# Kernel tuning notes

Measured on AMD Instinct MI355X. Metric: run time of the kernel, lower is better.

## Reference

```python
import jax, jax.numpy as jnp
import numpy as np

B, H, L, D, LBL = 512, 64, 528, 32, 10
NI = 64          # number of interval breakpoints
W = 128          # vf MLP width
N_STEPS = 256    # fixed Tsit5 steps over [t0, t1]

# Tsit5 Butcher tableau
C2, C3, C4, C5, C6 = 0.161, 0.327, 0.9, 0.9800255409045097, 1.0
A21 = 0.161
A31, A32 = -0.008480655492356989, 0.335480655492357
A41, A42, A43 = 2.8971530571054935, -6.359448489975075, 4.3622954328695815
A51, A52, A53, A54 = 5.325864828439257, -11.748883564062828, 7.4955393428898365, -0.09249506636175525
A61, A62, A63, A64, A65 = 5.86145544294642, -12.92096931784711, 8.159367898576159, -0.071584973281401, -0.028269050394068383
B1, B2, B3, B4, B5, B6 = 0.09646076681806523, 0.01, 0.4798896504144996, 1.379008574103742, -3.290069515436081, 2.324710524099774


def _linear_init(k, out_dim, in_dim):
    lim = 1.0 / np.sqrt(in_dim)
    kw, kb = jax.random.split(k)
    w = jax.random.uniform(kw, (out_dim, in_dim), jnp.float32, -lim, lim)
    b = jax.random.uniform(kb, (out_dim,), jnp.float32, -lim, lim)
    return w, b


def setup_inputs() -> dict:
    key = jax.random.key(0)
    ks = jax.random.split(key, 8)
    ts = jnp.linspace(0.0, 1.0, 129, dtype=jnp.float32)
    logsig = 0.1 * jax.random.normal(ks[0], (B, NI + 1, L + 1), jnp.float32)
    x0 = jax.random.normal(ks[1], (B, D), jnp.float32)
    intervals = jnp.linspace(0.0, 1.0, NI, dtype=jnp.float32)
    vf_w0, vf_b0 = _linear_init(ks[2], W, H)
    vf_w1, vf_b1 = _linear_init(ks[3], W, W)
    vf_w2, vf_b2 = _linear_init(ks[4], W, W)
    vf_w3, vf_b3 = _linear_init(ks[5], H * L, W)
    l1_w, l1_b = _linear_init(ks[6], H, D)
    l2_w, l2_b = _linear_init(ks[7], LBL, H)
    return dict(ts=ts, logsig=logsig, x0=x0, intervals=intervals,
                vf_w0=vf_w0, vf_b0=vf_b0, vf_w1=vf_w1, vf_b1=vf_b1,
                vf_w2=vf_w2, vf_b2=vf_b2, vf_w3=vf_w3, vf_b3=vf_b3,
                l1_w=l1_w, l1_b=l1_b, l2_w=l2_w, l2_b=l2_b)


def reference(ts, logsig, x0, intervals,
              vf_w0, vf_b0, vf_w1, vf_b1, vf_w2, vf_b2, vf_w3, vf_b3,
              l1_w, l1_b, l2_w, l2_b):
    Bn = x0.shape[0]
    Hn = l1_w.shape[0]
    Ln = vf_b3.shape[0] // Hn

    def vf(y):  # y: (B, H) -> (B, H, L)
        h = jax.nn.silu(y @ vf_w0.T + vf_b0)
        h = jax.nn.silu(h @ vf_w1.T + vf_b1)
        h = jax.nn.silu(h @ vf_w2.T + vf_b2)
        out = jnp.tanh(h @ vf_w3.T + vf_b3)
        return out.reshape(Bn, Hn, Ln)

    def func(t, y):
        idx = jnp.searchsorted(intervals, t)
        sig = logsig[:, idx, 1:]          # (B, L)
        return jnp.einsum('bhl,bl->bh', vf(y), sig)

    t0, t1 = ts[0], ts[-1]
    dt = (t1 - t0) / N_STEPS

    def step(y, i):
        t = t0 + i * dt
        k1 = func(t, y)
        k2 = func(t + C2 * dt, y + dt * (A21 * k1))
        k3 = func(t + C3 * dt, y + dt * (A31 * k1 + A32 * k2))
        k4 = func(t + C4 * dt, y + dt * (A41 * k1 + A42 * k2 + A43 * k3))
        k5 = func(t + C5 * dt, y + dt * (A51 * k1 + A52 * k2 + A53 * k3 + A54 * k4))
        k6 = func(t + C6 * dt, y + dt * (A61 * k1 + A62 * k2 + A63 * k3 + A64 * k4 + A65 * k5))
        y_new = y + dt * (B1 * k1 + B2 * k2 + B3 * k3 + B4 * k4 + B5 * k5 + B6 * k6)
        return y_new, None

    y0 = x0 @ l1_w.T + l1_b
    yT, _ = jax.lax.scan(step, y0, jnp.arange(N_STEPS, dtype=jnp.float32))
    return jax.nn.softmax(yT @ l2_w.T + l2_b, axis=-1)
```

## Files before the change

kernel.cpp:

```cpp
#include <hip/hip_runtime.h>
#include <stdint.h>

#define NBLK 256
#define NTHR 512

typedef __attribute__((ext_vector_type(8))) short short8;
typedef __attribute__((ext_vector_type(4))) float float4_;

#define WS_BAR  0
#define WS_HDNF 16384
#define WS_KF   (16384 + 131072)

#define LOADC(p)    __hip_atomic_load((p),  __ATOMIC_RELAXED, __HIP_MEMORY_SCOPE_SYSTEM)
#define STOREC(p,v) __hip_atomic_store((p), (v), __ATOMIC_RELAXED, __HIP_MEMORY_SCOPE_SYSTEM)

__device__ __forceinline__ unsigned short f2bf(float x) {
  union { float f; unsigned u; } v; v.f = x;
  return (unsigned short)((v.u + 0x7fffu + ((v.u >> 16) & 1u)) >> 16);
}
__device__ __forceinline__ float fast_exp(float x) {
  return __builtin_amdgcn_exp2f(x * 1.4426950408889634f);
}
__device__ __forceinline__ float fast_tanh(float x) {
  float e = __builtin_amdgcn_exp2f(x * 2.8853900817779268f);
  return fmaf(-2.0f, __builtin_amdgcn_rcpf(e + 1.0f), 1.0f);
}
__device__ __forceinline__ float fast_silu(float x) {
  float e = fast_exp(-x);
  return x * __builtin_amdgcn_rcpf(1.0f + e);
}

__device__ __forceinline__ void rgbar(unsigned* bar, int h, int Rg, unsigned bn) {
  __syncthreads();
  if (threadIdx.x == 0) {
    unsigned* base = bar + 32 * (32 + Rg * 16);
    unsigned* leaf = base + 32 * (h & 7);
    unsigned* root = base + 32 * 8;
    unsigned* gen  = base + 32 * 9;
    unsigned a = __hip_atomic_fetch_add(leaf, 1u, __ATOMIC_RELAXED, __HIP_MEMORY_SCOPE_SYSTEM);
    if (a == 8u * bn - 1u) {
      unsigned r = __hip_atomic_fetch_add(root, 1u, __ATOMIC_RELAXED, __HIP_MEMORY_SCOPE_SYSTEM);
      if (r == 8u * bn - 1u) STOREC(gen, bn);
    }
    while (LOADC(gen) < bn) __builtin_amdgcn_s_sleep(1);
  }
  __syncthreads();
}

template<int SIN>
__device__ __forceinline__ void rk_stage(
    int stepi, int sg, int g, int h, int Rg, int R,
    float (&kh)[6], float& y, float t0v, float dtv,
    unsigned char* ws, unsigned* BAR, unsigned& rseq,
    const float* logsig, const float* w0, const float* b0,
    const float* w1, const float* b1, const float* w2, const float* b2,
    unsigned short* w3lds, float* b3lds, float* intv,
    float (*yst)[64], float (*hb1)[128], float (*hb2)[128],
    unsigned short (*hdnS)[128], int* sidxp) {
  const int tid = threadIdx.x;
  const int lane = tid & 63, wv = tid >> 6;
  const int col = lane & 15, qd = lane >> 4;
  unsigned* HDNF = (unsigned*)(ws + WS_HDNF);
  float* KF  = (float*)(ws + WS_KF);

  if (sg > 0 && tid < 128) {
    const float* KFr = KF + ((sg & 1) ^ 1) * 32768;
    constexpr int pi = (SIN == 0) ? 5 : SIN - 1;
    kh[pi] = LOADC(&KFr[(size_t)(2 * g + (tid >> 6)) * 64 + (tid & 63)]);
  }
  if (tid < 128) {
    float ystv;
    if constexpr (SIN == 0) {
      if (sg > 0) {
        y += dtv * (0.09646076681806523f * kh[0] + 0.01f * kh[1]
                  + 0.4798896504144996f * kh[2] + 1.379008574103742f * kh[3]
                  - 3.290069515436081f * kh[4] + 2.324710524099774f * kh[5]);
      }
      ystv = y;
    } else if constexpr (SIN == 1) {
      ystv = y + dtv * (0.161f * kh[0]);
    } else if constexpr (SIN == 2) {
      ystv = y + dtv * (-0.008480655492356989f * kh[0] + 0.335480655492357f * kh[1]);
    } else if constexpr (SIN == 3) {
      ystv = y + dtv * (2.8971530571054935f * kh[0] - 6.359448489975075f * kh[1]
                      + 4.3622954328695815f * kh[2]);
    } else if constexpr (SIN == 4) {
      ystv = y + dtv * (5.325864828439257f * kh[0] - 11.748883564062828f * kh[1]
                      + 7.4955393428898365f * kh[2] - 0.09249506636175525f * kh[3]);
    } else {
      ystv = y + dtv * (5.86145544294642f * kh[0] - 12.92096931784711f * kh[1]
                      + 8.159367898576159f * kh[2] - 0.071584973281401f * kh[3]
                      - 0.028269050394068383f * kh[4]);
    }
    yst[tid >> 6][tid & 63] = ystv;
  }
  {
    float tb = __fadd_rn(t0v, __fmul_rn((float)stepi, dtv));
    float t_cur;
    if constexpr (SIN == 0) t_cur = tb;
    else {
      constexpr float cS = (SIN == 1) ? 0.161f : (SIN == 2) ? 0.327f : (SIN == 3) ? 0.9f
                         : (SIN == 4) ? 0.9800255409045097f : 1.0f;
      t_cur = __fadd_rn(tb, __fmul_rn(cS, dtv));
    }
    if (tid < 64) {
      unsigned long long m1 = __ballot(intv[tid] < t_cur);
      if (tid == 0) *sidxp = (int)__popcll(m1);
    }
  }
  __syncthreads();
  const int idx = *sidxp;

  if (tid < 256) {
    const int row = tid >> 7, j = tid & 127;
    const float4_* wr = (const float4_*)(w0 + (size_t)j * 64);
    float ac[4] = {b0[j], 0.0f, 0.0f, 0.0f};
    #pragma unroll
    for (int i4 = 0; i4 < 16; ++i4) {
      float4_ wvv = wr[i4];
      float s = fmaf(yst[row][4*i4+0], wvv[0], yst[row][4*i4+1] * wvv[1]);
      s = fmaf(yst[row][4*i4+2], wvv[2], s);
      s = fmaf(yst[row][4*i4+3], wvv[3], s);
      ac[i4 & 3] += s;
    }
    hb1[row][j] = fast_silu((ac[0] + ac[1]) + (ac[2] + ac[3]));
  }
  __syncthreads();
  if (tid < 256) {
    const int row = tid >> 7, j = tid & 127;
    const float4_* wr = (const float4_*)(w1 + (size_t)j * 128);
    float ac[4] = {b1[j], 0.0f, 0.0f, 0.0f};
    #pragma unroll
    for (int i4 = 0; i4 < 32; ++i4) {
      float4_ wvv = wr[i4];
      float s = fmaf(hb1[row][4*i4+0], wvv[0], hb1[row][4*i4+1] * wvv[1]);
      s = fmaf(hb1[row][4*i4+2], wvv[2], s);
      s = fmaf(hb1[row][4*i4+3], wvv[3], s);
      ac[i4 & 3] += s;
    }
    hb2[row][j] = fast_silu((ac[0] + ac[1]) + (ac[2] + ac[3]));
  }
  __syncthreads();
  if (tid < 256) {
    const int row = tid >> 7, j = tid & 127;
    const float4_* wr = (const float4_*)(w2 + (size_t)j * 128);
    float ac[4] = {b2[j], 0.0f, 0.0f, 0.0f};
    #pragma unroll
    for (int i4 = 0; i4 < 32; ++i4) {
      float4_ wvv = wr[i4];
      float s = fmaf(hb2[row][4*i4+0], wvv[0], hb2[row][4*i4+1] * wvv[1]);
      s = fmaf(hb2[row][4*i4+2], wvv[2], s);
      s = fmaf(hb2[row][4*i4+3], wvv[3], s);
      ac[i4 & 3] += s;
    }
    hdnS[row][j] = f2bf(fast_silu((ac[0] + ac[1]) + (ac[2] + ac[3])));
  }
  __syncthreads();
  if (tid < 128) {
    const int row = tid >> 6, u = tid & 63;
    const int lb = 2 * h + row;
    const int tile = lb >> 4, colp = lb & 15;
    const int j0 = 2 * u;
    const int kb = j0 >> 5, qdp = (j0 >> 3) & 3, jj = j0 & 7;
    unsigned v = (unsigned)hdnS[row][j0] | ((unsigned)hdnS[row][j0 + 1] << 16);
    unsigned i16 = (unsigned)((Rg * 32 + tile * 4 + kb) * 512 + qdp * 128 + colp * 8 + jj);
    STOREC(&HDNF[i16 >> 1], v);
  }
  ++rseq; rgbar(BAR, h, Rg, rseq);

  {
    const unsigned long long* H64 = (const unsigned long long*)HDNF;
    union { unsigned long long u[2]; short8 s; } af[4];
    #pragma unroll
    for (int kb = 0; kb < 4; ++kb) {
      const unsigned i16 = (unsigned)((Rg * 32 + wv * 4 + kb) * 512 + lane * 8);
      af[kb].u[0] = LOADC(&H64[i16 >> 2]);
      af[kb].u[1] = LOADC(&H64[(i16 >> 2) + 1]);
    }
    const float* sp0 = logsig + (size_t)(R + wv * 16 + qd * 4) * 34385 + (size_t)idx * 529 + 1;
    const float* sp1 = sp0 + 34385;
    const float* sp2 = sp0 + 2 * 34385;
    const float* sp3 = sp0 + 3 * 34385;
    float kp[4] = {0.0f, 0.0f, 0.0f, 0.0f};
    #pragma unroll 2
    for (int nt = 0; nt < 33; ++nt) {
      const int l = nt * 16 + col;
      const float bv = b3lds[l];
      float4_ acc; acc[0] = bv; acc[1] = bv; acc[2] = bv; acc[3] = bv;
      #pragma unroll
      for (int kb = 0; kb < 4; ++kb) {
        const short8 bf = *(const short8*)(w3lds + ((nt * 4 + kb) * 64 + lane) * 8);
        acc = __builtin_amdgcn_mfma_f32_16x16x32_bf16(af[kb].s, bf, acc, 0, 0, 0);
      }
      kp[0] = fmaf(fast_tanh(acc[0]), sp0[l], kp[0]);
      kp[1] = fmaf(fast_tanh(acc[1]), sp1[l], kp[1]);
      kp[2] = fmaf(fast_tanh(acc[2]), sp2[l], kp[2]);
      kp[3] = fmaf(fast_tanh(acc[3]), sp3[l], kp[3]);
    }
    #pragma unroll
    for (int r = 0; r < 4; ++r) {
      float v = kp[r];
      v += __shfl_xor(v, 1); v += __shfl_xor(v, 2);
      v += __shfl_xor(v, 4); v += __shfl_xor(v, 8);
      kp[r] = v;
    }
    if (col == 0) {
      float* KFw = KF + (sg & 1) * 32768;
      #pragma unroll
      for (int r = 0; r < 4; ++r)
        STOREC(&KFw[(size_t)(R + wv * 16 + qd * 4 + r) * 64 + h], kp[r]);
    }
  }
  ++rseq; rgbar(BAR, h, Rg, rseq);
}

__global__ void __launch_bounds__(NTHR, 2)
rde_kernel(const float* __restrict__ ts, const float* __restrict__ logsig,
           const float* __restrict__ x0, const float* __restrict__ intervals,
           const float* __restrict__ w0, const float* __restrict__ b0,
           const float* __restrict__ w1, const float* __restrict__ b1,
           const float* __restrict__ w2, const float* __restrict__ b2,
           const float* __restrict__ w3, const float* __restrict__ b3,
           const float* __restrict__ l1w, const float* __restrict__ l1b,
           const float* __restrict__ l2w, const float* __restrict__ l2b,
           float* out, unsigned char* ws) {
  const int tid = threadIdx.x;
  const int g = blockIdx.x;
  const int h = g & 63;
  const int Rg = g >> 6;
  const int R = Rg * 128;
  unsigned* BAR = (unsigned*)(ws + WS_BAR);
  unsigned rseq = 0;

  __shared__ __attribute__((aligned(16))) unsigned short w3lds[67584];
  __shared__ float b3lds[528];
  __shared__ float intv[64];
  __shared__ float yst[2][64];
  __shared__ float hb1[2][128];
  __shared__ float hb2[2][128];
  __shared__ __attribute__((aligned(8))) unsigned short hdnS[2][128];
  __shared__ int sidx;

  if (tid < 64) intv[tid] = intervals[tid];
  for (int e = tid; e < 528; e += NTHR) b3lds[e] = b3[(size_t)h * 528 + e];

  for (int e = tid; e < 8448; e += NTHR) {
    const int ln = e & 63, kb = (e >> 6) & 3, nt = e >> 8;
    const float* src = w3 + ((size_t)(h * 528 + nt * 16 + (ln & 15))) * 128 + kb * 32 + (ln >> 4) * 8;
    union { unsigned short s[8]; short8 v; } p;
    #pragma unroll
    for (int j = 0; j < 8; ++j) p.s[j] = f2bf(src[j]);
    *(short8*)(w3lds + e * 8) = p.v;
  }

  float y = 0.0f, kh[6];
  #pragma unroll
  for (int i = 0; i < 6; ++i) kh[i] = 0.0f;
  if (tid < 128) {
    const int row = tid >> 6, hh = tid & 63;
    float acc = l1b[hh];
    const float4_* xr = (const float4_*)(x0 + (size_t)(2 * g + row) * 32);
    const float4_* wr = (const float4_*)(l1w + (size_t)hh * 32);
    #pragma unroll
    for (int d = 0; d < 8; ++d) {
      float4_ xv = xr[d], wvv = wr[d];
      acc = fmaf(xv[0], wvv[0], acc); acc = fmaf(xv[1], wvv[1], acc);
      acc = fmaf(xv[2], wvv[2], acc); acc = fmaf(xv[3], wvv[3], acc);
    }
    y = acc;
  }
  const float t0v = ts[0];
  const float dtv = (ts[128] - t0v) * (1.0f / 256.0f);
  __syncthreads();

  for (int stepi = 0; stepi < 256; ++stepi) {
    const int sg = stepi * 6;
    rk_stage<0>(stepi, sg + 0, g, h, Rg, R, kh, y, t0v, dtv, ws, BAR, rseq,
                logsig, w0, b0, w1, b1, w2, b2, w3lds, b3lds, intv, yst, hb1, hb2, hdnS, &sidx);
    rk_stage<1>(stepi, sg + 1, g, h, Rg, R, kh, y, t0v, dtv, ws, BAR, rseq,
                logsig, w0, b0, w1, b1, w2, b2, w3lds, b3lds, intv, yst, hb1, hb2, hdnS, &sidx);
    rk_stage<2>(stepi, sg + 2, g, h, Rg, R, kh, y, t0v, dtv, ws, BAR, rseq,
                logsig, w0, b0, w1, b1, w2, b2, w3lds, b3lds, intv, yst, hb1, hb2, hdnS, &sidx);
    rk_stage<3>(stepi, sg + 3, g, h, Rg, R, kh, y, t0v, dtv, ws, BAR, rseq,
                logsig, w0, b0, w1, b1, w2, b2, w3lds, b3lds, intv, yst, hb1, hb2, hdnS, &sidx);
    rk_stage<4>(stepi, sg + 4, g, h, Rg, R, kh, y, t0v, dtv, ws, BAR, rseq,
                logsig, w0, b0, w1, b1, w2, b2, w3lds, b3lds, intv, yst, hb1, hb2, hdnS, &sidx);
    rk_stage<5>(stepi, sg + 5, g, h, Rg, R, kh, y, t0v, dtv, ws, BAR, rseq,
                logsig, w0, b0, w1, b1, w2, b2, w3lds, b3lds, intv, yst, hb1, hb2, hdnS, &sidx);
  }

  {
    float* KF = (float*)(ws + WS_KF);
    if (tid < 128) {
      const int row = tid >> 6, hh = tid & 63;
      kh[5] = LOADC(&KF[(size_t)32768 + (size_t)(2 * g + row) * 64 + hh]);
      y += dtv * (0.09646076681806523f * kh[0] + 0.01f * kh[1]
                + 0.4798896504144996f * kh[2] + 1.379008574103742f * kh[3]
                - 3.290069515436081f * kh[4] + 2.324710524099774f * kh[5]);
      yst[row][hh] = y;
    }
    __syncthreads();
    if (tid < 20) {
      const int row = tid / 10, c = tid % 10;
      float acc = l2b[c];
      const float* wr = l2w + c * 64;
      #pragma unroll
      for (int i2 = 0; i2 < 64; ++i2) acc = fmaf(yst[row][i2], wr[i2], acc);
      hb1[row][c] = acc;
    }
    __syncthreads();
    if (tid < 2) {
      const int row = tid;
      float mx = -1e30f;
      for (int c = 0; c < 10; ++c) mx = fmaxf(mx, hb1[row][c]);
      float ev[10], den = 0.0f;
      for (int c = 0; c < 10; ++c) { ev[c] = expf(hb1[row][c] - mx); den += ev[c]; }
      const float rd = 1.0f / den;
      for (int c = 0; c < 10; ++c) out[(size_t)(2 * g + row) * 10 + c] = ev[c] * rd;
    }
  }
}

extern "C" void kernel_launch(void* const* d_in, const int* in_sizes, int n_in,
                              void* d_out, int out_size, void* d_ws, size_t ws_size,
                              hipStream_t stream) {
  (void)in_sizes; (void)n_in; (void)out_size; (void)ws_size;
  const float* ts        = (const float*)d_in[0];
  const float* logsig    = (const float*)d_in[1];
  const float* x0        = (const float*)d_in[2];
  const float* intervals = (const float*)d_in[3];
  const float* w0        = (const float*)d_in[4];
  const float* b0        = (const float*)d_in[5];
  const float* w1        = (const float*)d_in[6];
  const float* b1        = (const float*)d_in[7];
  const float* w2        = (const float*)d_in[8];
  const float* b2        = (const float*)d_in[9];
  const float* w3        = (const float*)d_in[10];
  const float* b3        = (const float*)d_in[11];
  const float* l1w       = (const float*)d_in[12];
  const float* l1b       = (const float*)d_in[13];
  const float* l2w       = (const float*)d_in[14];
  const float* l2b       = (const float*)d_in[15];
  float* out = (float*)d_out;
  unsigned char* ws = (unsigned char*)d_ws;

  hipMemsetAsync(d_ws, 0, 12288, stream);

  void* args[] = { &ts, &logsig, &x0, &intervals, &w0, &b0, &w1, &b1,
                   &w2, &b2, &w3, &b3, &l1w, &l1b, &l2w, &l2b, &out, &ws };
  hipLaunchCooperativeKernel((void*)rde_kernel, dim3(NBLK), dim3(NTHR), args, 0, stream);
}
```

Baseline: 36.38 ms.

## Keep MLP hidden-layer weights in registers and split dot products across all threads

The w1 and w2 rows each thread needs are loaded once into registers before the time loop, so the global/L2 weight reads inside every RK stage go away. The first three MLP layers now use all 512 threads, with each output split into two half-dot-products joined by a cross-lane shuffle. Block-to-(row group, head) mapping is also permuted, likely to place blocks sharing a barrier group together. The trade-off is higher register pressure, which could cause spills under the 2-blocks-per-CU launch bound, plus a shuffle per layer.

```diff
diff --git a/kernel.cpp b/kernel.cpp
--- a/kernel.cpp
+++ b/kernel.cpp
@@ -49,24 +49,26 @@
 
 template<int SIN>
 __device__ __forceinline__ void rk_stage(
-    int stepi, int sg, int g, int h, int Rg, int R,
+    int stepi, int sg, int h, int Rg, int R, int r0,
     float (&kh)[6], float& y, float t0v, float dtv,
+    const float4_ (&wr1)[16], const float4_ (&wr2)[16],
+    float b0r, float b1r, float b2r,
     unsigned char* ws, unsigned* BAR, unsigned& rseq,
-    const float* logsig, const float* w0, const float* b0,
-    const float* w1, const float* b1, const float* w2, const float* b2,
+    const float* logsig, const float* w0,
     unsigned short* w3lds, float* b3lds, float* intv,
     float (*yst)[64], float (*hb1)[128], float (*hb2)[128],
     unsigned short (*hdnS)[128], int* sidxp) {
   const int tid = threadIdx.x;
   const int lane = tid & 63, wv = tid >> 6;
   const int col = lane & 15, qd = lane >> 4;
+  const int mrow = tid >> 8, mj = ((tid >> 6) & 3) * 32 + (tid & 31), mhalf = (tid >> 5) & 1;
   unsigned* HDNF = (unsigned*)(ws + WS_HDNF);
   float* KF  = (float*)(ws + WS_KF);
 
   if (sg > 0 && tid < 128) {
     const float* KFr = KF + ((sg & 1) ^ 1) * 32768;
     constexpr int pi = (SIN == 0) ? 5 : SIN - 1;
-    kh[pi] = LOADC(&KFr[(size_t)(2 * g + (tid >> 6)) * 64 + (tid & 63)]);
+    kh[pi] = LOADC(&KFr[(size_t)(r0 + (tid >> 6)) * 64 + (tid & 63)]);
   }
   if (tid < 128) {
     float ystv;
@@ -111,49 +113,53 @@
   __syncthreads();
   const int idx = *sidxp;
 
-  if (tid < 256) {
-    const int row = tid >> 7, j = tid & 127;
-    const float4_* wr = (const float4_*)(w0 + (size_t)j * 64);
-    float ac[4] = {b0[j], 0.0f, 0.0f, 0.0f};
+  {
+    const float4_* wrp = (const float4_*)(w0 + (size_t)mj * 64 + mhalf * 32);
+    const float* yp = &yst[mrow][mhalf * 32];
+    float ac0 = 0.0f, ac1 = 0.0f;
+    #pragma unroll
+    for (int i4 = 0; i4 < 8; ++i4) {
+      float4_ wvv = wrp[i4];
+      float s = fmaf(yp[4*i4+0], wvv[0], yp[4*i4+1] * wvv[1]);
+      s = fmaf(yp[4*i4+2], wvv[2], s);
+      s = fmaf(yp[4*i4+3], wvv[3], s);
+      if (i4 & 1) ac1 += s; else ac0 += s;
+    }
+    float v = ac0 + ac1;
+    v += __shfl_xor(v, 32);
+    if (mhalf == 0) hb1[mrow][mj] = fast_silu(v + b0r);
+  }
+  __syncthreads();
+  {
+    const float* hp = &hb1[mrow][mhalf * 64];
+    float ac0 = 0.0f, ac1 = 0.0f;
     #pragma unroll
     for (int i4 = 0; i4 < 16; ++i4) {
-      float4_ wvv = wr[i4];
-      float s = fmaf(yst[row][4*i4+0], wvv[0], yst[row][4*i4+1] * wvv[1]);
-      s = fmaf(yst[row][4*i4+2], wvv[2], s);
-      s = fmaf(yst[row][4*i4+3], wvv[3], s);
-      ac[i4 & 3] += s;
-    }
-    hb1[row][j] = fast_silu((ac[0] + ac[1]) + (ac[2] + ac[3]));
-  }
-  __syncthreads();
-  if (tid < 256) {
-    const int row = tid >> 7, j = tid & 127;
-    const float4_* wr = (const float4_*)(w1 + (size_t)j * 128);
-    float ac[4] = {b1[j], 0.0f, 0.0f, 0.0f};
-    #pragma unroll
-    for (int i4 = 0; i4 < 32; ++i4) {
-      float4_ wvv = wr[i4];
-      float s = fmaf(hb1[row][4*i4+0], wvv[0], hb1[row][4*i4+1] * wvv[1]);
-      s = fmaf(hb1[row][4*i4+2], wvv[2], s);
-      s = fmaf(hb1[row][4*i4+3], wvv[3], s);
-      ac[i4 & 3] += s;
-    }
-    hb2[row][j] = fast_silu((ac[0] + ac[1]) + (ac[2] + ac[3]));
-  }
-  __syncthreads();
-  if (tid < 256) {
-    const int row = tid >> 7, j = tid & 127;
-    const float4_* wr = (const float4_*)(w2 + (size_t)j * 128);
-    float ac[4] = {b2[j], 0.0f, 0.0f, 0.0f};
-    #pragma unroll
-    for (int i4 = 0; i4 < 32; ++i4) {
-      float4_ wvv = wr[i4];
-      float s = fmaf(hb2[row][4*i4+0], wvv[0], hb2[row][4*i4+1] * wvv[1]);
-      s = fmaf(hb2[row][4*i4+2], wvv[2], s);
-      s = fmaf(hb2[row][4*i4+3], wvv[3], s);
-      ac[i4 & 3] += s;
-    }
-    hdnS[row][j] = f2bf(fast_silu((ac[0] + ac[1]) + (ac[2] + ac[3])));
+      float4_ wvv = wr1[i4];
+      float s = fmaf(hp[4*i4+0], wvv[0], hp[4*i4+1] * wvv[1]);
+      s = fmaf(hp[4*i4+2], wvv[2], s);
+      s = fmaf(hp[4*i4+3], wvv[3], s);
+      if (i4 & 1) ac1 += s; else ac0 += s;
+    }
+    float v = ac0 + ac1;
+    v += __shfl_xor(v, 32);
+    if (mhalf == 0) hb2[mrow][mj] = fast_silu(v + b1r);
+  }
+  __syncthreads();
+  {
+    const float* hp = &hb2[mrow][mhalf * 64];
+    float ac0 = 0.0f, ac1 = 0.0f;
+    #pragma unroll
+    for (int i4 = 0; i4 < 16; ++i4) {
+      float4_ wvv = wr2[i4];
+      float s = fmaf(hp[4*i4+0], wvv[0], hp[4*i4+1] * wvv[1]);
+      s = fmaf(hp[4*i4+2], wvv[2], s);
+      s = fmaf(hp[4*i4+3], wvv[3], s);
+      if (i4 & 1) ac1 += s; else ac0 += s;
+    }
+    float v = ac0 + ac1;
+    v += __shfl_xor(v, 32);
+    if (mhalf == 0) hdnS[mrow][mj] = f2bf(fast_silu(v + b2r));
   }
   __syncthreads();
   if (tid < 128) {
@@ -226,9 +232,10 @@
            float* out, unsigned char* ws) {
   const int tid = threadIdx.x;
   const int g = blockIdx.x;
-  const int h = g & 63;
-  const int Rg = g >> 6;
+  const int Rg = (g >> 1) & 3;
+  const int h  = ((g >> 3) << 1) | (g & 1);
   const int R = Rg * 128;
+  const int r0 = R + 2 * h;
   unsigned* BAR = (unsigned*)(ws + WS_BAR);
   unsigned rseq = 0;
 
@@ -253,13 +260,23 @@
     *(short8*)(w3lds + e * 8) = p.v;
   }
 
+  const int mj = ((tid >> 6) & 3) * 32 + (tid & 31), mhalf = (tid >> 5) & 1;
+  float4_ wr1[16], wr2[16];
+  {
+    const float4_* s1 = (const float4_*)(w1 + (size_t)mj * 128 + mhalf * 64);
+    const float4_* s2 = (const float4_*)(w2 + (size_t)mj * 128 + mhalf * 64);
+    #pragma unroll
+    for (int i = 0; i < 16; ++i) { wr1[i] = s1[i]; wr2[i] = s2[i]; }
+  }
+  const float b0r = b0[mj], b1r = b1[mj], b2r = b2[mj];
+
   float y = 0.0f, kh[6];
   #pragma unroll
   for (int i = 0; i < 6; ++i) kh[i] = 0.0f;
   if (tid < 128) {
     const int row = tid >> 6, hh = tid & 63;
     float acc = l1b[hh];
-    const float4_* xr = (const float4_*)(x0 + (size_t)(2 * g + row) * 32);
+    const float4_* xr = (const float4_*)(x0 + (size_t)(r0 + row) * 32);
     const float4_* wr = (const float4_*)(l1w + (size_t)hh * 32);
     #pragma unroll
     for (int d = 0; d < 8; ++d) {
@@ -275,25 +292,25 @@
 
   for (int stepi = 0; stepi < 256; ++stepi) {
     const int sg = stepi * 6;
-    rk_stage<0>(stepi, sg + 0, g, h, Rg, R, kh, y, t0v, dtv, ws, BAR, rseq,
-                logsig, w0, b0, w1, b1, w2, b2, w3lds, b3lds, intv, yst, hb1, hb2, hdnS, &sidx);
-    rk_stage<1>(stepi, sg + 1, g, h, Rg, R, kh, y, t0v, dtv, ws, BAR, rseq,
-                logsig, w0, b0, w1, b1, w2, b2, w3lds, b3lds, intv, yst, hb1, hb2, hdnS, &sidx);
-    rk_stage<2>(stepi, sg + 2, g, h, Rg, R, kh, y, t0v, dtv, ws, BAR, rseq,
-                logsig, w0, b0, w1, b1, w2, b2, w3lds, b3lds, intv, yst, hb1, hb2, hdnS, &sidx);
-    rk_stage<3>(stepi, sg + 3, g, h, Rg, R, kh, y, t0v, dtv, ws, BAR, rseq,
-                logsig, w0, b0, w1, b1, w2, b2, w3lds, b3lds, intv, yst, hb1, hb2, hdnS, &sidx);
-    rk_stage<4>(stepi, sg + 4, g, h, Rg, R, kh, y, t0v, dtv, ws, BAR, rseq,
-                logsig, w0, b0, w1, b1, w2, b2, w3lds, b3lds, intv, yst, hb1, hb2, hdnS, &sidx);
-    rk_stage<5>(stepi, sg + 5, g, h, Rg, R, kh, y, t0v, dtv, ws, BAR, rseq,
-                logsig, w0, b0, w1, b1, w2, b2, w3lds, b3lds, intv, yst, hb1, hb2, hdnS, &sidx);
+    rk_stage<0>(stepi, sg + 0, h, Rg, R, r0, kh, y, t0v, dtv, wr1, wr2, b0r, b1r, b2r,
+                ws, BAR, rseq, logsig, w0, w3lds, b3lds, intv, yst, hb1, hb2, hdnS, &sidx);
+    rk_stage<1>(stepi, sg + 1, h, Rg, R, r0, kh, y, t0v, dtv, wr1, wr2, b0r, b1r, b2r,
+                ws, BAR, rseq, logsig, w0, w3lds, b3lds, intv, yst, hb1, hb2, hdnS, &sidx);
+    rk_stage<2>(stepi, sg + 2, h, Rg, R, r0, kh, y, t0v, dtv, wr1, wr2, b0r, b1r, b2r,
+                ws, BAR, rseq, logsig, w0, w3lds, b3lds, intv, yst, hb1, hb2, hdnS, &sidx);
+    rk_stage<3>(stepi, sg + 3, h, Rg, R, r0, kh, y, t0v, dtv, wr1, wr2, b0r, b1r, b2r,
+                ws, BAR, rseq, logsig, w0, w3lds, b3lds, intv, yst, hb1, hb2, hdnS, &sidx);
+    rk_stage<4>(stepi, sg + 4, h, Rg, R, r0, kh, y, t0v, dtv, wr1, wr2, b0r, b1r, b2r,
+                ws, BAR, rseq, logsig, w0, w3lds, b3lds, intv, yst, hb1, hb2, hdnS, &sidx);
+    rk_stage<5>(stepi, sg + 5, h, Rg, R, r0, kh, y, t0v, dtv, wr1, wr2, b0r, b1r, b2r,
+                ws, BAR, rseq, logsig, w0, w3lds, b3lds, intv, yst, hb1, hb2, hdnS, &sidx);
   }
 
   {
     float* KF = (float*)(ws + WS_KF);
     if (tid < 128) {
       const int row = tid >> 6, hh = tid & 63;
-      kh[5] = LOADC(&KF[(size_t)32768 + (size_t)(2 * g + row) * 64 + hh]);
+      kh[5] = LOADC(&KF[(size_t)32768 + (size_t)(r0 + row) * 64 + hh]);
       y += dtv * (0.09646076681806523f * kh[0] + 0.01f * kh[1]
                 + 0.4798896504144996f * kh[2] + 1.379008574103742f * kh[3]
                 - 3.290069515436081f * kh[4] + 2.324710524099774f * kh[5]);
@@ -316,7 +333,7 @@
       float ev[10], den = 0.0f;
       for (int c = 0; c < 10; ++c) { ev[c] = expf(hb1[row][c] - mx); den += ev[c]; }
       const float rd = 1.0f / den;
-      for (int c = 0; c < 10; ++c) out[(size_t)(2 * g + row) * 10 + c] = ev[c] * rd;
+      for (int c = 0; c < 10; ++c) out[(size_t)(r0 + row) * 10 + c] = ev[c] * rd;
     }
   }
 }
```

After: 42.98 ms. +18.1%, slower.
